# Performance work log

Measured on AMD Instinct MI355X. Metric: run time of the kernel, lower is better.

Reference implementation:

```python
import jax, jax.numpy as jnp
import numpy as np
from math import sqrt

B, H, S, D = 4, 16, 2048, 64
NEG = -1000000000.0

def setup_inputs() -> dict:
    key = jax.random.key(0)
    kq, kk, kv, km = jax.random.split(key, 4)
    Q = jax.random.normal(kq, (B, H, S, D), dtype=jnp.float32)
    K = jax.random.normal(kk, (B, H, S, D), dtype=jnp.float32)
    V = jax.random.normal(kv, (B, H, S, D), dtype=jnp.float32)
    mask = jax.random.uniform(km, (B, 1, S, S)) < 0.1
    return {"Q": Q, "K": K, "V": V, "mask": mask}

def reference(Q, K, V, mask) -> jnp.ndarray:
    # scores: [B,H,S,S]
    scores = jnp.einsum('bhqd,bhkd->bhqk', Q, K)
    scores = jnp.where(mask, NEG, scores)
    attn = jax.nn.softmax(scores / sqrt(Q.shape[-1]), axis=-1)
    return jnp.einsum('bhqk,bhkd->bhqd', attn, V)
```

## Files before the change

### kernel.cpp

```cpp
#include <hip/hip_runtime.h>


#define SEQ 2048
#define DIM 64
#define NBH 64
#define LOG2E 1.44269504088896340736f
#define SCL (0.125f * LOG2E)
#define NEG_SCALED -1.25e8f

typedef short bf16x8 __attribute__((ext_vector_type(8)));
typedef float f32x4 __attribute__((ext_vector_type(4)));
typedef float f32x16 __attribute__((ext_vector_type(16)));

static __device__ __forceinline__ unsigned short f2bf(float f) {
    unsigned int u = __float_as_uint(f);
    u += 0x7fffu + ((u >> 16) & 1u);
    return (unsigned short)(u >> 16);
}

#define GLD16(gp, lp) __builtin_amdgcn_global_load_lds( \
    (const __attribute__((address_space(1))) unsigned int*)(gp), \
    (__attribute__((address_space(3))) unsigned int*)(lp), 16, 0, 0)

__global__ __launch_bounds__(256)
void prep_all_kernel(const float* __restrict__ K, const float* __restrict__ V,
                     const int* __restrict__ M,
                     unsigned short* __restrict__ Kb, unsigned short* __restrict__ Vt,
                     unsigned int* __restrict__ Mpt) {
    const int x = blockIdx.x;
    const int t = threadIdx.x;
    if (x < 4096) {
        size_t i0 = ((size_t)x * 256 + t) * 8;
        float4 a = *(const float4*)(K + i0);
        float4 b = *(const float4*)(K + i0 + 4);
        union { uint4 u; unsigned short s[8]; } w;
        w.s[0] = f2bf(a.x); w.s[1] = f2bf(a.y); w.s[2] = f2bf(a.z); w.s[3] = f2bf(a.w);
        w.s[4] = f2bf(b.x); w.s[5] = f2bf(b.y); w.s[6] = f2bf(b.z); w.s[7] = f2bf(b.w);
        *(uint4*)(Kb + i0) = w.u;
    } else if (x < 6144) {
        __shared__ __align__(16) unsigned short T[64 * 64];
        const int vb = x - 4096;
        const int bh = vb >> 5;
        const int k0 = (vb & 31) * 64;
        {
            const int kk = t >> 2;
            const int c  = t & 3;
            const int cs = c ^ ((kk >> 3) & 3);
            const float* vp = V + ((size_t)bh * SEQ + k0 + kk) * DIM + c * 16;
            union { uint4 u[2]; unsigned short s[16]; } w;
            #pragma unroll
            for (int j = 0; j < 16; ++j) w.s[j] = f2bf(vp[j]);
            *(uint4*)&T[kk * 64 + cs * 16]     = w.u[0];
            *(uint4*)&T[kk * 64 + cs * 16 + 8] = w.u[1];
        }
        __syncthreads();
        {
            const int kc = t & 7;
            const int dp = t >> 3;
            const int ch = (dp >> 3) ^ (kc & 3);
            const unsigned int* T32 = (const unsigned int*)T;
            union { uint4 u; unsigned short s[8]; } o0, o1;
            #pragma unroll
            for (int i = 0; i < 8; ++i) {
                unsigned int v = T32[(8 * kc + i) * 32 + ch * 8 + (dp & 7)];
                o0.s[i] = (unsigned short)v;
                o1.s[i] = (unsigned short)(v >> 16);
            }
            unsigned short* op = Vt + ((size_t)bh * DIM + 2 * dp) * SEQ + k0 + 8 * kc;
            *(uint4*)op         = o0.u;
            *(uint4*)(op + SEQ) = o1.u;
        }
    } else {
        const int g = (x - 6144) * 256 + t;
        const int b = g >> 17;
        const int r = g & 131071;
        const int q = r >> 6;
        const int it = r & 63;
        const int4* p = (const int4*)(M + (((size_t)b * SEQ + q) * SEQ + it * 32));
        unsigned int m = 0;
        #pragma unroll
        for (int j = 0; j < 8; ++j) {
            int4 v = p[j];
            m |= (unsigned int)(v.x != 0) << (4 * j);
            m |= (unsigned int)(v.y != 0) << (4 * j + 1);
            m |= (unsigned int)(v.z != 0) << (4 * j + 2);
            m |= (unsigned int)(v.w != 0) << (4 * j + 3);
        }
        Mpt[((size_t)b * 64 + it) * SEQ + q] = m;
    }
}

__global__ __launch_bounds__(256, 4)
void attn_main_kernel(const float* __restrict__ Q,
                      const unsigned short* __restrict__ Kb,
                      const unsigned short* __restrict__ Vt,
                      const unsigned int* __restrict__ Mpt,
                      float* __restrict__ O)
{
    const int bh   = blockIdx.y;
    const int b    = bh >> 4;
    const int q0   = blockIdx.x * 128;
    const int tid  = threadIdx.x;
    const int wave = tid >> 6;
    const int lane = tid & 63;
    const int h    = lane >> 5;
    const int q32  = lane & 31;

    __shared__ __align__(16) unsigned short Kt[2][32 * 64];
    __shared__ __align__(16) unsigned short Vs[2][64 * 32];

    const unsigned short* Kbh = Kb + (size_t)bh * SEQ * DIM;
    const unsigned short* Vbh = Vt + (size_t)bh * SEQ * DIM;

    bf16x8 qf[4];
    {
        const float* qp = Q + ((size_t)bh * SEQ + q0 + wave * 32 + q32) * DIM + h * 8;
        #pragma unroll
        for (int dc = 0; dc < 4; ++dc) {
            float4 xx = *(const float4*)(qp + dc * 16);
            float4 yy = *(const float4*)(qp + dc * 16 + 4);
            qf[dc][0] = (short)f2bf(xx.x * SCL); qf[dc][1] = (short)f2bf(xx.y * SCL);
            qf[dc][2] = (short)f2bf(xx.z * SCL); qf[dc][3] = (short)f2bf(xx.w * SCL);
            qf[dc][4] = (short)f2bf(yy.x * SCL); qf[dc][5] = (short)f2bf(yy.y * SCL);
            qf[dc][6] = (short)f2bf(yy.z * SCL); qf[dc][7] = (short)f2bf(yy.w * SCL);
        }
    }

    const int kkey  = wave * 8 + (lane >> 3);
    const int kclog = (lane & 7) ^ (lane >> 3);
    const unsigned short* kg = Kbh + (size_t)kkey * DIM + kclog * 8;
    const int vd    = wave * 16 + (lane >> 2);
    const int vclog = (lane & 3) ^ ((lane >> 2) & 3);
    const unsigned short* vg = Vbh + (size_t)vd * SEQ + vclog * 8;
    unsigned short* kl[2] = { &Kt[0][wave * 512], &Kt[1][wave * 512] };
    unsigned short* vl[2] = { &Vs[0][wave * 512], &Vs[1][wave * 512] };

    const unsigned int* mp = Mpt + (size_t)b * 64 * SEQ + (q0 + wave * 32 + q32);

    f32x16 acc[2];
    #pragma unroll
    for (int i = 0; i < 16; ++i) { acc[0][i] = 0.f; acc[1][i] = 0.f; }
    float lsum = 0.f;

    GLD16(kg, kl[0]);
    GLD16(vg, vl[0]);

    #pragma unroll 2
    for (int it = 0; it < SEQ / 32; ++it) {
        __syncthreads();

        unsigned int mw = mp[it * SEQ];

        if (it + 1 < SEQ / 32) {
            const unsigned short* kgn = kg + (size_t)(it + 1) * 32 * DIM;
            const unsigned short* vgn = vg + (size_t)(it + 1) * 32;
            int nb = (it + 1) & 1;
            GLD16(kgn, kl[nb]);
            GLD16(vgn, vl[nb]);
        }

        const unsigned short* Ktb = Kt[it & 1];
        const unsigned short* Vsb = Vs[it & 1];

        f32x16 sc;
        #pragma unroll
        for (int i = 0; i < 16; ++i) sc[i] = 0.f;
        #pragma unroll
        for (int dc = 0; dc < 4; ++dc) {
            const int pos = (dc * 2 + h) ^ (q32 & 7);
            bf16x8 kf = *(const bf16x8*)(Ktb + q32 * 64 + pos * 8);
            sc = __builtin_amdgcn_mfma_f32_32x32x16_bf16(kf, qf[dc], sc, 0, 0, 0);
        }

        const unsigned int mq = mw >> (4 * h);
        float pv[16];
        #pragma unroll
        for (int r = 0; r < 16; ++r) {
            const int s = (r & 3) + 8 * (r >> 2);
            float e = __builtin_amdgcn_exp2f(sc[r]);
            pv[r] = ((mq >> s) & 1u) ? 0.f : e;
            lsum += pv[r];
        }
        unsigned int pk[8];
        #pragma unroll
        for (int m = 0; m < 8; ++m) {
            unsigned int u0 = __float_as_uint(pv[2 * m])     + 0x8000u;
            unsigned int u1 = __float_as_uint(pv[2 * m + 1]) + 0x8000u;
            pk[m] = __builtin_amdgcn_perm(u1, u0, 0x07060302u);
        }

        #pragma unroll
        for (int kk = 0; kk < 2; ++kk) {
            unsigned int s0 = h ? pk[4 * kk + 0] : pk[4 * kk + 2];
            unsigned int s1 = h ? pk[4 * kk + 1] : pk[4 * kk + 3];
            unsigned int r0 = (unsigned int)__shfl_xor((int)s0, 32);
            unsigned int r1 = (unsigned int)__shfl_xor((int)s1, 32);
            union { unsigned int u[4]; bf16x8 v; } fr;
            fr.u[0] = h ? r0 : pk[4 * kk + 0];
            fr.u[1] = h ? r1 : pk[4 * kk + 1];
            fr.u[2] = h ? pk[4 * kk + 2] : r0;
            fr.u[3] = h ? pk[4 * kk + 3] : r1;

            #pragma unroll
            for (int dh = 0; dh < 2; ++dh) {
                const int d   = dh * 32 + q32;
                const int pos = (kk * 2 + h) ^ (d & 3);
                bf16x8 vf = *(const bf16x8*)(Vsb + d * 32 + pos * 8);
                acc[dh] = __builtin_amdgcn_mfma_f32_32x32x16_bf16(vf, fr.v, acc[dh], 0, 0, 0);
            }
        }
    }

    lsum += __shfl_xor(lsum, 32);
    const float inv = 1.f / lsum;
    float* orow = O + ((size_t)bh * SEQ + q0 + wave * 32 + q32) * DIM;
    #pragma unroll
    for (int dh = 0; dh < 2; ++dh) {
        #pragma unroll
        for (int r23 = 0; r23 < 4; ++r23) {
            float4 w;
            w.x = acc[dh][4 * r23 + 0] * inv;
            w.y = acc[dh][4 * r23 + 1] * inv;
            w.z = acc[dh][4 * r23 + 2] * inv;
            w.w = acc[dh][4 * r23 + 3] * inv;
            *(float4*)(orow + dh * 32 + r23 * 8 + h * 4) = w;
        }
    }
}

__global__ __launch_bounds__(256)
void attn_fallback_kernel(const float* __restrict__ Q,
                          const float* __restrict__ K,
                          const float* __restrict__ V,
                          const int* __restrict__ mask,
                          float* __restrict__ O)
{
    const int bh   = blockIdx.y;
    const int b    = bh >> 4;
    const int q0   = blockIdx.x * 64;
    const int tid  = threadIdx.x;
    const int wave = tid >> 6;
    const int lane = tid & 63;
    const int quad = lane >> 4;
    const int l16  = lane & 15;

    __shared__ __align__(16) unsigned short Klds[32][72];
    __shared__ __align__(16) unsigned short VT[64][40];
    __shared__ __align__(16) unsigned short Plds[4][16][40];

    const float* Qb = Q + (size_t)bh * SEQ * DIM;
    const float* Kb = K + (size_t)bh * SEQ * DIM;
    const float* Vb = V + (size_t)bh * SEQ * DIM;
    const int*   Mb = mask + (size_t)b * SEQ * SEQ;

    const int qrow_frag = q0 + wave * 16 + l16;
    bf16x8 qf0, qf1;
    {
        const float* qp = Qb + (size_t)qrow_frag * DIM + quad * 8;
        #pragma unroll
        for (int i = 0; i < 8; ++i) {
            qf0[i] = (short)f2bf(qp[i]);
            qf1[i] = (short)f2bf(qp[32 + i]);
        }
    }

    f32x4 acc[4];
    #pragma unroll
    for (int dg = 0; dg < 4; ++dg) acc[dg] = (f32x4){0.f, 0.f, 0.f, 0.f};
    float mrowv[4] = {-INFINITY, -INFINITY, -INFINITY, -INFINITY};
    float lrow[4] = {0.f, 0.f, 0.f, 0.f};

    const int skey = tid >> 3;
    const int sd0  = (tid & 7) * 8;
    const int vkey = tid & 31;
    const int vd0  = (tid >> 5) * 8;
    const int qrow_m = q0 + wave * 16 + quad * 4;

    for (int kb = 0; kb < SEQ; kb += 32) {
        __syncthreads();
        {
            const float* kp = Kb + (size_t)(kb + skey) * DIM + sd0;
            union { uint4 u4; unsigned short s[8]; } kw;
            #pragma unroll
            for (int i = 0; i < 8; ++i) kw.s[i] = f2bf(kp[i]);
            *(uint4*)&Klds[skey][sd0] = kw.u4;
        }
        {
            const float* vp = Vb + (size_t)(kb + vkey) * DIM + vd0;
            #pragma unroll
            for (int i = 0; i < 8; ++i) VT[vd0 + i][vkey] = f2bf(vp[i]);
        }
        __syncthreads();

        f32x4 scr[2];
        scr[0] = (f32x4){0.f, 0.f, 0.f, 0.f};
        scr[1] = (f32x4){0.f, 0.f, 0.f, 0.f};
        #pragma unroll
        for (int nt = 0; nt < 2; ++nt) {
            bf16x8 kf0 = *(const bf16x8*)&Klds[nt * 16 + l16][quad * 8];
            bf16x8 kf1 = *(const bf16x8*)&Klds[nt * 16 + l16][32 + quad * 8];
            scr[nt] = __builtin_amdgcn_mfma_f32_16x16x32_bf16(qf0, kf0, scr[nt], 0, 0, 0);
            scr[nt] = __builtin_amdgcn_mfma_f32_16x16x32_bf16(qf1, kf1, scr[nt], 0, 0, 0);
        }

        float x[2][4];
        #pragma unroll
        for (int nt = 0; nt < 2; ++nt)
            #pragma unroll
            for (int r = 0; r < 4; ++r) {
                int mv = Mb[(size_t)(qrow_m + r) * SEQ + kb + nt * 16 + l16];
                x[nt][r] = mv ? NEG_SCALED : scr[nt][r] * 0.125f;
            }

        float p[2][4];
        #pragma unroll
        for (int r = 0; r < 4; ++r) {
            float rm = fmaxf(x[0][r], x[1][r]);
            #pragma unroll
            for (int off = 1; off < 16; off <<= 1)
                rm = fmaxf(rm, __shfl_xor(rm, off, 16));
            float mn = fmaxf(mrowv[r], rm);
            float alpha = exp2f((mrowv[r] - mn) * LOG2E);
            mrowv[r] = mn;
            float p0 = exp2f((x[0][r] - mn) * LOG2E);
            float p1 = exp2f((x[1][r] - mn) * LOG2E);
            p[0][r] = p0; p[1][r] = p1;
            float rs = p0 + p1;
            #pragma unroll
            for (int off = 1; off < 16; off <<= 1)
                rs += __shfl_xor(rs, off, 16);
            lrow[r] = lrow[r] * alpha + rs;
            #pragma unroll
            for (int dg = 0; dg < 4; ++dg)
                acc[dg][r] *= alpha;
        }

        #pragma unroll
        for (int nt = 0; nt < 2; ++nt)
            #pragma unroll
            for (int r = 0; r < 4; ++r)
                Plds[wave][quad * 4 + r][nt * 16 + l16] = f2bf(p[nt][r]);

        bf16x8 pf = *(const bf16x8*)&Plds[wave][l16][quad * 8];

        #pragma unroll
        for (int dg = 0; dg < 4; ++dg) {
            bf16x8 vf = *(const bf16x8*)&VT[dg * 16 + l16][quad * 8];
            acc[dg] = __builtin_amdgcn_mfma_f32_16x16x32_bf16(pf, vf, acc[dg], 0, 0, 0);
        }
    }

    float* Ob = O + (size_t)bh * SEQ * DIM;
    #pragma unroll
    for (int r = 0; r < 4; ++r) {
        float inv = 1.f / lrow[r];
        #pragma unroll
        for (int dg = 0; dg < 4; ++dg)
            Ob[(size_t)(qrow_m + r) * DIM + dg * 16 + l16] = acc[dg][r] * inv;
    }
}

extern "C" void kernel_launch(void* const* d_in, const int* in_sizes, int n_in,
                              void* d_out, int out_size, void* d_ws, size_t ws_size,
                              hipStream_t stream) {
    const float* Q = (const float*)d_in[0];
    const float* K = (const float*)d_in[1];
    const float* V = (const float*)d_in[2];
    const int* mask = (const int*)d_in[3];
    float*        O = (float*)d_out;

    const size_t szK = (size_t)NBH * SEQ * DIM * 2;
    const size_t szV = (size_t)NBH * SEQ * DIM * 2;
    const size_t szM = (size_t)4 * SEQ * (SEQ / 32) * 4;
    const size_t need = szK + szV + szM;

    if (ws_size >= need) {
        unsigned short* Kb = (unsigned short*)d_ws;
        unsigned short* Vt = (unsigned short*)((char*)d_ws + szK);
        unsigned int*  Mpt = (unsigned int*)((char*)d_ws + szK + szV);

        prep_all_kernel<<<dim3(8192), 256, 0, stream>>>(K, V, mask, Kb, Vt, Mpt);
        attn_main_kernel<<<dim3(SEQ / 128, NBH), 256, 0, stream>>>(Q, Kb, Vt, Mpt, O);
    } else {
        attn_fallback_kernel<<<dim3(SEQ / 64, NBH), 256, 0, stream>>>(Q, K, V, mask, O);
    }
}
```

Before: 290.7 us.

## Permute V key order to drop cross-half shuffles and coalesce mask packing

The V transpose prep now permutes key rows within 16-row groups so that each lane's packed P values already match the MFMA B-operand layout. This removes the two cross-half __shfl_xor exchanges and selects per k-step in the main loop, and changes the LDS swizzle for the V tile to match. The mask-packing path is restructured so each wave reads whole rows with coalesced int4 loads, combines nibbles with lane shuffles, and transposes through shared memory before writing, which reduces the prep grid. It risks subtle layout mismatches between the prep permutation and the consumer's swizzle.

```diff
diff --git a/kernel.cpp b/kernel.cpp
--- a/kernel.cpp
+++ b/kernel.cpp
@@ -45,13 +45,14 @@
         {
             const int kk = t >> 2;
             const int c  = t & 3;
-            const int cs = c ^ ((kk >> 3) & 3);
+            const int u  = (kk & ~12) | ((kk & 4) << 1) | ((kk & 8) >> 1);
+            const int cs = c ^ ((u >> 3) & 3);
             const float* vp = V + ((size_t)bh * SEQ + k0 + kk) * DIM + c * 16;
-            union { uint4 u[2]; unsigned short s[16]; } w;
+            union { uint4 q[2]; unsigned short s[16]; } w;
             #pragma unroll
             for (int j = 0; j < 16; ++j) w.s[j] = f2bf(vp[j]);
-            *(uint4*)&T[kk * 64 + cs * 16]     = w.u[0];
-            *(uint4*)&T[kk * 64 + cs * 16 + 8] = w.u[1];
+            *(uint4*)&T[u * 64 + cs * 16]     = w.q[0];
+            *(uint4*)&T[u * 64 + cs * 16 + 8] = w.q[1];
         }
         __syncthreads();
         {
@@ -71,22 +72,33 @@
             *(uint4*)(op + SEQ) = o1.u;
         }
     } else {
-        const int g = (x - 6144) * 256 + t;
-        const int b = g >> 17;
-        const int r = g & 131071;
-        const int q = r >> 6;
-        const int it = r & 63;
-        const int4* p = (const int4*)(M + (((size_t)b * SEQ + q) * SEQ + it * 32));
-        unsigned int m = 0;
-        #pragma unroll
-        for (int j = 0; j < 8; ++j) {
-            int4 v = p[j];
-            m |= (unsigned int)(v.x != 0) << (4 * j);
-            m |= (unsigned int)(v.y != 0) << (4 * j + 1);
-            m |= (unsigned int)(v.z != 0) << (4 * j + 2);
-            m |= (unsigned int)(v.w != 0) << (4 * j + 3);
-        }
-        Mpt[((size_t)b * 64 + it) * SEQ + q] = m;
+        __shared__ unsigned int Wt[64][8];
+        const int m  = x - 6144;
+        const int b  = m >> 8;
+        const int q0 = ((m >> 3) & 31) * 64;
+        const int k0 = (m & 7) * 256;
+        const int w  = t >> 6, l = t & 63;
+        #pragma unroll 4
+        for (int row = 0; row < 16; ++row) {
+            const int q = q0 + w * 16 + row;
+            int4 v4 = *(const int4*)(M + ((size_t)b * SEQ + q) * SEQ + k0 + l * 4);
+            unsigned int nib = (unsigned int)(v4.x != 0) | ((unsigned int)(v4.y != 0) << 1)
+                             | ((unsigned int)(v4.z != 0) << 2) | ((unsigned int)(v4.w != 0) << 3);
+            unsigned int v = nib << (4 * (l & 7));
+            v |= __shfl_xor(v, 1);
+            v |= __shfl_xor(v, 2);
+            v |= __shfl_xor(v, 4);
+            if ((l & 7) == 0) Wt[w * 16 + row][l >> 3] = v;
+        }
+        __syncthreads();
+        {
+            const int q = t & 63, g0 = t >> 6;
+            #pragma unroll
+            for (int gg = 0; gg < 2; ++gg) {
+                const int g = g0 + gg * 4;
+                Mpt[((size_t)b * 64 + (k0 >> 5) + g) * SEQ + q0 + q] = Wt[q][g];
+            }
+        }
     }
 }
 
@@ -130,7 +142,7 @@
     const int kclog = (lane & 7) ^ (lane >> 3);
     const unsigned short* kg = Kbh + (size_t)kkey * DIM + kclog * 8;
     const int vd    = wave * 16 + (lane >> 2);
-    const int vclog = (lane & 3) ^ ((lane >> 2) & 3);
+    const int vclog = (lane & 3) ^ ((lane >> 3) & 3);
     const unsigned short* vg = Vbh + (size_t)vd * SEQ + vclog * 8;
     unsigned short* kl[2] = { &Kt[0][wave * 512], &Kt[1][wave * 512] };
     unsigned short* vl[2] = { &Vs[0][wave * 512], &Vs[1][wave * 512] };
@@ -191,20 +203,15 @@
 
         #pragma unroll
         for (int kk = 0; kk < 2; ++kk) {
-            unsigned int s0 = h ? pk[4 * kk + 0] : pk[4 * kk + 2];
-            unsigned int s1 = h ? pk[4 * kk + 1] : pk[4 * kk + 3];
-            unsigned int r0 = (unsigned int)__shfl_xor((int)s0, 32);
-            unsigned int r1 = (unsigned int)__shfl_xor((int)s1, 32);
             union { unsigned int u[4]; bf16x8 v; } fr;
-            fr.u[0] = h ? r0 : pk[4 * kk + 0];
-            fr.u[1] = h ? r1 : pk[4 * kk + 1];
-            fr.u[2] = h ? pk[4 * kk + 2] : r0;
-            fr.u[3] = h ? pk[4 * kk + 3] : r1;
-
+            fr.u[0] = pk[4 * kk + 0];
+            fr.u[1] = pk[4 * kk + 1];
+            fr.u[2] = pk[4 * kk + 2];
+            fr.u[3] = pk[4 * kk + 3];
             #pragma unroll
             for (int dh = 0; dh < 2; ++dh) {
                 const int d   = dh * 32 + q32;
-                const int pos = (kk * 2 + h) ^ (d & 3);
+                const int pos = (kk * 2 + h) ^ ((q32 >> 1) & 3);
                 bf16x8 vf = *(const bf16x8*)(Vsb + d * 32 + pos * 8);
                 acc[dh] = __builtin_amdgcn_mfma_f32_32x32x16_bf16(vf, fr.v, acc[dh], 0, 0, 0);
             }
@@ -379,7 +386,7 @@
         unsigned short* Vt = (unsigned short*)((char*)d_ws + szK);
         unsigned int*  Mpt = (unsigned int*)((char*)d_ws + szK + szV);
 
-        prep_all_kernel<<<dim3(8192), 256, 0, stream>>>(K, V, mask, Kb, Vt, Mpt);
+        prep_all_kernel<<<dim3(7168), 256, 0, stream>>>(K, V, mask, Kb, Vt, Mpt);
         attn_main_kernel<<<dim3(SEQ / 128, NBH), 256, 0, stream>>>(Q, Kb, Vt, Mpt, O);
     } else {
         attn_fallback_kernel<<<dim3(SEQ / 64, NBH), 256, 0, stream>>>(Q, K, V, mask, O);
```

Measured after the change: 277.7 us. 4.5% less time.
